# Performance work log

Measured on AMD Instinct MI355X. Metric: run time of the kernel, lower is better.

Reference implementation:

```python
import jax, jax.numpy as jnp
import numpy as np

NUM_EMBEDDINGS = 1024
EMBEDDING_DIM = 64

def setup_inputs() -> dict:
    key = jax.random.key(0)
    k1, k2 = jax.random.split(key)
    x = jax.random.normal(k1, (16, 64, 64, EMBEDDING_DIM), dtype=jnp.float32)
    # tf.random_uniform_initializer default: U(-0.05, 0.05)
    embeddings = jax.random.uniform(k2, (EMBEDDING_DIM, NUM_EMBEDDINGS),
                                    dtype=jnp.float32, minval=-0.05, maxval=0.05)
    return {"x": x, "embeddings": embeddings}

def reference(x, embeddings):
    input_shape = x.shape
    D = embeddings.shape[0]
    flat = x.reshape(-1, D)  # [N, D]
    # squared L2 distances: ||z||^2 + ||e||^2 - 2 z.e
    similarity = flat @ embeddings  # [N, K]
    distances = (jnp.sum(flat * flat, axis=1, keepdims=True)
                 + jnp.sum(embeddings * embeddings, axis=0)
                 - 2.0 * similarity)
    indices = jnp.argmin(distances, axis=1)  # [N]
    # one-hot @ embeddings.T == gather rows of embeddings.T
    quantized = jnp.take(embeddings.T, indices, axis=0)  # [N, D]
    return quantized.reshape(input_shape)
```

## Files before the change

### kernel.cpp

```cpp
#include <hip/hip_runtime.h>
#include <float.h>

#define K_CODES 1024
#define DIM 64
#define BR 128
#define SAFE_MARGIN 2.5e-4f

typedef __attribute__((ext_vector_type(8))) short bf16x8;
typedef __attribute__((ext_vector_type(8))) unsigned short u16x8;
typedef __attribute__((ext_vector_type(4))) float f32x4;

__device__ __forceinline__ unsigned short f2bf(float f) {
    unsigned int u = __float_as_uint(f);
    u += 0x7fff + ((u >> 16) & 1);
    return (unsigned short)(u >> 16);
}
__device__ __forceinline__ float bf2f(unsigned short h) {
    return __uint_as_float(((unsigned int)h) << 16);
}
__device__ __forceinline__ int swz(int row, int byteInRow) {
    return row * 128 + (byteInRow ^ ((row & 7) << 4));
}

__global__ __launch_bounds__(256) void vq_prep2(
    const float* __restrict__ E, float* __restrict__ Et,
    unsigned short* __restrict__ Eh, unsigned short* __restrict__ El,
    float* __restrict__ nrm, int* __restrict__ cnt)
{
    __shared__ float T[64 * 17];
    const int t = threadIdx.x;
    const int k0 = blockIdx.x * 16;
    if (blockIdx.x == 0 && t == 0) *cnt = 0;
    #pragma unroll
    for (int i = 0; i < 4; ++i) {
        int idx = i * 256 + t;
        int d = idx >> 4, kk = idx & 15;
        T[d * 17 + kk] = E[d * K_CODES + k0 + kk];
    }
    __syncthreads();
    #pragma unroll
    for (int i = 0; i < 4; ++i) {
        int idx = i * 256 + t;
        int kk = idx >> 6, d = idx & 63;
        float v = T[d * 17 + kk];
        Et[(size_t)(k0 + kk) * DIM + d] = v;
        unsigned short h = f2bf(v);
        Eh[(size_t)(k0 + kk) * DIM + d] = h;
        El[(size_t)(k0 + kk) * DIM + d] = f2bf(v - bf2f(h));
    }
    if (t < 16) {
        float s = 0.f;
        #pragma unroll
        for (int d = 0; d < DIM; ++d) {
            float v = T[d * 17 + t];
            s = __builtin_fmaf(v, v, s);
        }
        nrm[k0 + t] = s;
    }
}

__global__ __launch_bounds__(256, 2) void vq_mfma(
    const float* __restrict__ x,
    const unsigned short* __restrict__ Eh,
    const unsigned short* __restrict__ El,
    const float* __restrict__ nrm,
    const float* __restrict__ Et,
    float* __restrict__ out,
    int* __restrict__ cnt, int* __restrict__ list)
{
    __shared__ char lds[66048];
    char* Ah = lds;
    char* Al = lds + 16384;
    char* Bh = lds + 32768;
    char* Bl = lds + 49152;
    int* bidx = (int*)(lds + 65536);

    const int t    = threadIdx.x;
    const int lane = t & 63;
    const int wv   = t >> 6;
    const int col  = lane & 15;
    const int q    = lane >> 4;
    const int koff = q * 16;
    const long r0  = (long)blockIdx.x * BR;

    {
        int row = t >> 1, h = t & 1;
        const float4* src = (const float4*)(x + (r0 + row) * DIM + h * 32);
        float v[32];
        #pragma unroll
        for (int i = 0; i < 8; ++i) {
            float4 f = src[i];
            v[4*i+0] = f.x; v[4*i+1] = f.y; v[4*i+2] = f.z; v[4*i+3] = f.w;
        }
        unsigned short hi[32], lo[32];
        #pragma unroll
        for (int i = 0; i < 32; ++i) {
            hi[i] = f2bf(v[i]);
            lo[i] = f2bf(v[i] - bf2f(hi[i]));
        }
        #pragma unroll
        for (int s = 0; s < 2; ++s) {
            int seg = h * 2 + s;
            *(u16x8*)(Ah + swz(row, seg*32))      = *(u16x8*)(hi + s*16);
            *(u16x8*)(Ah + swz(row, seg*32 + 16)) = *(u16x8*)(hi + s*16 + 8);
            *(u16x8*)(Al + swz(row, seg*32))      = *(u16x8*)(lo + s*16);
            *(u16x8*)(Al + swz(row, seg*32 + 16)) = *(u16x8*)(lo + s*16 + 8);
        }
    }
    __syncthreads();

    bf16x8 aH[2][2], aL[2][2];
    #pragma unroll
    for (int m = 0; m < 2; ++m) {
        int arow = wv * 32 + m * 16 + col;
        #pragma unroll
        for (int kk = 0; kk < 2; ++kk) {
            aH[m][kk] = *(bf16x8*)(Ah + swz(arow, kk*64 + koff));
            aL[m][kk] = *(bf16x8*)(Al + swz(arow, kk*64 + koff));
        }
    }

    float b1[2][4], b2[2][4];
    int   i1[2][4];
    #pragma unroll
    for (int m = 0; m < 2; ++m)
        #pragma unroll
        for (int j = 0; j < 4; ++j) { b1[m][j] = FLT_MAX; b2[m][j] = FLT_MAX; i1[m][j] = 0x7fffffff; }

    for (int c0 = 0; c0 < K_CODES; c0 += 128) {
        __syncthreads();
        #pragma unroll
        for (int i = 0; i < 4; ++i) {
            int idx = i * 256 + t;
            int cr = idx >> 3, sg = idx & 7;
            *(u16x8*)(Bh + swz(cr, sg*16)) = *(const u16x8*)(Eh + (size_t)(c0+cr)*DIM + sg*8);
            *(u16x8*)(Bl + swz(cr, sg*16)) = *(const u16x8*)(El + (size_t)(c0+cr)*DIM + sg*8);
        }
        __syncthreads();

        #pragma unroll
        for (int nt = 0; nt < 8; ++nt) {
            int brow = nt * 16 + col;
            bf16x8 bH0 = *(bf16x8*)(Bh + swz(brow, koff));
            bf16x8 bH1 = *(bf16x8*)(Bh + swz(brow, 64 + koff));
            bf16x8 bL0 = *(bf16x8*)(Bl + swz(brow, koff));
            bf16x8 bL1 = *(bf16x8*)(Bl + swz(brow, 64 + koff));
            int code = c0 + nt * 16 + col;
            float ne = nrm[code];
            #pragma unroll
            for (int m = 0; m < 2; ++m) {
                f32x4 acc = {0.f, 0.f, 0.f, 0.f};
                acc = __builtin_amdgcn_mfma_f32_16x16x32_bf16(aH[m][0], bH0, acc, 0,0,0);
                acc = __builtin_amdgcn_mfma_f32_16x16x32_bf16(aH[m][1], bH1, acc, 0,0,0);
                acc = __builtin_amdgcn_mfma_f32_16x16x32_bf16(aH[m][0], bL0, acc, 0,0,0);
                acc = __builtin_amdgcn_mfma_f32_16x16x32_bf16(aH[m][1], bL1, acc, 0,0,0);
                acc = __builtin_amdgcn_mfma_f32_16x16x32_bf16(aL[m][0], bH0, acc, 0,0,0);
                acc = __builtin_amdgcn_mfma_f32_16x16x32_bf16(aL[m][1], bH1, acc, 0,0,0);
                #pragma unroll
                for (int j = 0; j < 4; ++j) {
                    float dist = __builtin_fmaf(-2.f, acc[j], ne);
                    if (dist < b1[m][j]) { b2[m][j] = b1[m][j]; b1[m][j] = dist; i1[m][j] = code; }
                    else if (dist < b2[m][j]) { b2[m][j] = dist; }
                }
            }
        }
    }

    #pragma unroll
    for (int msk = 1; msk < 16; msk <<= 1) {
        #pragma unroll
        for (int m = 0; m < 2; ++m)
            #pragma unroll
            for (int j = 0; j < 4; ++j) {
                float o1 = __shfl_xor(b1[m][j], msk, 64);
                int   oi = __shfl_xor(i1[m][j], msk, 64);
                float o2 = __shfl_xor(b2[m][j], msk, 64);
                bool take = (o1 < b1[m][j]) || (o1 == b1[m][j] && oi < i1[m][j]);
                float worst = take ? b1[m][j] : o1;
                if (take) { b1[m][j] = o1; i1[m][j] = oi; }
                b2[m][j] = fminf(fminf(b2[m][j], o2), worst);
            }
    }
    if (col == 0) {
        #pragma unroll
        for (int m = 0; m < 2; ++m)
            #pragma unroll
            for (int j = 0; j < 4; ++j) {
                int rowl = wv * 32 + m * 16 + q * 4 + j;
                bidx[rowl] = i1[m][j];
                if (b2[m][j] - b1[m][j] <= SAFE_MARGIN) {
                    int p = atomicAdd(cnt, 1);
                    list[p] = (int)(r0 + rowl);
                }
            }
    }
    __syncthreads();

    {
        int rowl = t >> 1, h = t & 1;
        int code = bidx[rowl];
        const float4* src = (const float4*)(Et + (size_t)code * DIM + h * 32);
        float4* dst = (float4*)(out + (size_t)(r0 + rowl) * DIM + h * 32);
        #pragma unroll
        for (int i = 0; i < 8; ++i) dst[i] = src[i];
    }
}

__global__ __launch_bounds__(256) void vq_refine3(
    const float* __restrict__ x, const float* __restrict__ Et,
    const float* __restrict__ nrm, float* __restrict__ out,
    const int* __restrict__ cnt, const int* __restrict__ list)
{
    __shared__ float zsh[DIM];
    __shared__ float rv[4];
    __shared__ int   ri[4];
    __shared__ int   winner;
    const int n = *cnt;
    const int t = threadIdx.x;
    const int lane = t & 63, wv = t >> 6;

    for (int i = blockIdx.x; i < n; i += gridDim.x) {
        int row = list[i];
        if (t < DIM) zsh[t] = x[(size_t)row * DIM + t];
        __syncthreads();

        float zn = 0.f;
        #pragma unroll
        for (int d = 0; d < DIM; ++d) zn = __builtin_fmaf(zsh[d], zsh[d], zn);

        const float* e0 = Et + (size_t)(t      ) * DIM;
        const float* e1 = Et + (size_t)(t + 256) * DIM;
        const float* e2 = Et + (size_t)(t + 512) * DIM;
        const float* e3 = Et + (size_t)(t + 768) * DIM;
        float a0 = 0.f, a1 = 0.f, a2 = 0.f, a3 = 0.f;
        #pragma unroll
        for (int d = 0; d < DIM; ++d) {
            float zd = zsh[d];
            a0 = __builtin_fmaf(zd, e0[d], a0);
            a1 = __builtin_fmaf(zd, e1[d], a1);
            a2 = __builtin_fmaf(zd, e2[d], a2);
            a3 = __builtin_fmaf(zd, e3[d], a3);
        }
        float d0 = __builtin_fmaf(-2.f, a0, zn + nrm[t      ]);
        float d1 = __builtin_fmaf(-2.f, a1, zn + nrm[t + 256]);
        float d2 = __builtin_fmaf(-2.f, a2, zn + nrm[t + 512]);
        float d3 = __builtin_fmaf(-2.f, a3, zn + nrm[t + 768]);

        float b1 = d0; int i1v = t;
        if (d1 < b1) { b1 = d1; i1v = t + 256; }
        if (d2 < b1) { b1 = d2; i1v = t + 512; }
        if (d3 < b1) { b1 = d3; i1v = t + 768; }

        #pragma unroll
        for (int m = 1; m < 64; m <<= 1) {
            float o1 = __shfl_xor(b1, m, 64);
            int   oi = __shfl_xor(i1v, m, 64);
            if (o1 < b1 || (o1 == b1 && oi < i1v)) { b1 = o1; i1v = oi; }
        }
        if (lane == 0) { rv[wv] = b1; ri[wv] = i1v; }
        __syncthreads();
        if (t == 0) {
            float bv = rv[0]; int bi = ri[0];
            #pragma unroll
            for (int w = 1; w < 4; ++w)
                if (rv[w] < bv || (rv[w] == bv && ri[w] < bi)) { bv = rv[w]; bi = ri[w]; }
            winner = bi;
        }
        __syncthreads();
        if (t < DIM) out[(size_t)row * DIM + t] = Et[(size_t)winner * DIM + t];
        __syncthreads();
    }
}

extern "C" void kernel_launch(void* const* d_in, const int* in_sizes, int n_in,
                              void* d_out, int out_size, void* d_ws, size_t ws_size,
                              hipStream_t stream) {
    const float* x = (const float*)d_in[0];
    const float* E = (const float*)d_in[1];
    float* out = (float*)d_out;

    char* ws = (char*)d_ws;
    float*          Et   = (float*)ws;
    unsigned short* Eh   = (unsigned short*)(ws + 262144);
    unsigned short* El   = (unsigned short*)(ws + 393216);
    float*          nrm  = (float*)(ws + 524288);
    int*            cnt  = (int*)(ws + 528384);
    int*            list = (int*)(ws + 528640);

    int nrows = in_sizes[0] / DIM;

    vq_prep2<<<64, 256, 0, stream>>>(E, Et, Eh, El, nrm, cnt);
    vq_mfma<<<nrows / BR, 256, 0, stream>>>(x, Eh, El, nrm, Et, out, cnt, list);
    vq_refine3<<<512, 256, 0, stream>>>(x, Et, nrm, out, cnt, list);
}
```

Before: 131.2 us.

## Fuse refinement into MFMA kernel, alias LDS buffers, fold norm into accumulator

Removes the separate refine kernel and the global atomic list. Each block now keeps a per-block list of ambiguous rows in LDS and re-scores them in fp32 at the end. The B tiles reuse the A tile LDS space, halving shared memory so launch bounds can allow 4 blocks per CU, which needs a barrier reorganisation. The accumulator is seeded with half the code norm and x is negated, so the distance comes straight out of the MFMA, and the top-2 tracking uses fmin/fmed3 without branches. The risk is that a few blocks doing serial refinement become tail stragglers.

```diff
diff --git a/kernel.cpp b/kernel.cpp
--- a/kernel.cpp
+++ b/kernel.cpp
@@ -4,7 +4,7 @@
 #define K_CODES 1024
 #define DIM 64
 #define BR 128
-#define SAFE_MARGIN 2.5e-4f
+#define SAFE_MARGIN_H 1.25e-4f
 
 typedef __attribute__((ext_vector_type(8))) short bf16x8;
 typedef __attribute__((ext_vector_type(8))) unsigned short u16x8;
@@ -25,12 +25,11 @@
 __global__ __launch_bounds__(256) void vq_prep2(
     const float* __restrict__ E, float* __restrict__ Et,
     unsigned short* __restrict__ Eh, unsigned short* __restrict__ El,
-    float* __restrict__ nrm, int* __restrict__ cnt)
+    float* __restrict__ nrm, float* __restrict__ nrm2)
 {
     __shared__ float T[64 * 17];
     const int t = threadIdx.x;
     const int k0 = blockIdx.x * 16;
-    if (blockIdx.x == 0 && t == 0) *cnt = 0;
     #pragma unroll
     for (int i = 0; i < 4; ++i) {
         int idx = i * 256 + t;
@@ -55,25 +54,29 @@
             float v = T[d * 17 + t];
             s = __builtin_fmaf(v, v, s);
         }
-        nrm[k0 + t] = s;
-    }
-}
-
-__global__ __launch_bounds__(256, 2) void vq_mfma(
+        nrm [k0 + t] = s;
+        nrm2[k0 + t] = 0.5f * s;
+    }
+}
+
+__global__ __launch_bounds__(256, 4) void vq_mfma(
     const float* __restrict__ x,
+    const float* __restrict__ E,
     const unsigned short* __restrict__ Eh,
     const unsigned short* __restrict__ El,
     const float* __restrict__ nrm,
+    const float* __restrict__ nrm2,
     const float* __restrict__ Et,
-    float* __restrict__ out,
-    int* __restrict__ cnt, int* __restrict__ list)
+    float* __restrict__ out)
 {
-    __shared__ char lds[66048];
+    __shared__ char lds[32768 + 512 + 512 + 16];
     char* Ah = lds;
     char* Al = lds + 16384;
-    char* Bh = lds + 32768;
-    char* Bl = lds + 49152;
-    int* bidx = (int*)(lds + 65536);
+    char* Bh = lds;
+    char* Bl = lds + 16384;
+    int*  bidx  = (int*)(lds + 32768);
+    int*  flist = (int*)(lds + 33280);
+    int*  fcnt  = (int*)(lds + 33792);
 
     const int t    = threadIdx.x;
     const int lane = t & 63;
@@ -83,6 +86,8 @@
     const int koff = q * 16;
     const long r0  = (long)blockIdx.x * BR;
 
+    if (t == 0) *fcnt = 0;
+
     {
         int row = t >> 1, h = t & 1;
         const float4* src = (const float4*)(x + (r0 + row) * DIM + h * 32);
@@ -90,7 +95,7 @@
         #pragma unroll
         for (int i = 0; i < 8; ++i) {
             float4 f = src[i];
-            v[4*i+0] = f.x; v[4*i+1] = f.y; v[4*i+2] = f.z; v[4*i+3] = f.w;
+            v[4*i+0] = -f.x; v[4*i+1] = -f.y; v[4*i+2] = -f.z; v[4*i+3] = -f.w;
         }
         unsigned short hi[32], lo[32];
         #pragma unroll
@@ -119,6 +124,7 @@
             aL[m][kk] = *(bf16x8*)(Al + swz(arow, kk*64 + koff));
         }
     }
+    __syncthreads();
 
     float b1[2][4], b2[2][4];
     int   i1[2][4];
@@ -128,7 +134,6 @@
         for (int j = 0; j < 4; ++j) { b1[m][j] = FLT_MAX; b2[m][j] = FLT_MAX; i1[m][j] = 0x7fffffff; }
 
     for (int c0 = 0; c0 < K_CODES; c0 += 128) {
-        __syncthreads();
         #pragma unroll
         for (int i = 0; i < 4; ++i) {
             int idx = i * 256 + t;
@@ -146,10 +151,10 @@
             bf16x8 bL0 = *(bf16x8*)(Bl + swz(brow, koff));
             bf16x8 bL1 = *(bf16x8*)(Bl + swz(brow, 64 + koff));
             int code = c0 + nt * 16 + col;
-            float ne = nrm[code];
+            float ne2 = nrm2[code];
             #pragma unroll
             for (int m = 0; m < 2; ++m) {
-                f32x4 acc = {0.f, 0.f, 0.f, 0.f};
+                f32x4 acc = {ne2, ne2, ne2, ne2};
                 acc = __builtin_amdgcn_mfma_f32_16x16x32_bf16(aH[m][0], bH0, acc, 0,0,0);
                 acc = __builtin_amdgcn_mfma_f32_16x16x32_bf16(aH[m][1], bH1, acc, 0,0,0);
                 acc = __builtin_amdgcn_mfma_f32_16x16x32_bf16(aH[m][0], bL0, acc, 0,0,0);
@@ -158,12 +163,16 @@
                 acc = __builtin_amdgcn_mfma_f32_16x16x32_bf16(aL[m][1], bH1, acc, 0,0,0);
                 #pragma unroll
                 for (int j = 0; j < 4; ++j) {
-                    float dist = __builtin_fmaf(-2.f, acc[j], ne);
-                    if (dist < b1[m][j]) { b2[m][j] = b1[m][j]; b1[m][j] = dist; i1[m][j] = code; }
-                    else if (dist < b2[m][j]) { b2[m][j] = dist; }
+                    float d = acc[j];
+                    bool lt = d < b1[m][j];
+                    float nb1 = fminf(b1[m][j], d);
+                    b2[m][j] = __builtin_amdgcn_fmed3f(b1[m][j], b2[m][j], d);
+                    i1[m][j] = lt ? code : i1[m][j];
+                    b1[m][j] = nb1;
                 }
             }
         }
+        __syncthreads();
     }
 
     #pragma unroll
@@ -188,9 +197,9 @@
             for (int j = 0; j < 4; ++j) {
                 int rowl = wv * 32 + m * 16 + q * 4 + j;
                 bidx[rowl] = i1[m][j];
-                if (b2[m][j] - b1[m][j] <= SAFE_MARGIN) {
-                    int p = atomicAdd(cnt, 1);
-                    list[p] = (int)(r0 + rowl);
+                if (b2[m][j] - b1[m][j] <= SAFE_MARGIN_H) {
+                    int p = atomicAdd(fcnt, 1);
+                    flist[p] = rowl;
                 }
             }
     }
@@ -204,71 +213,58 @@
         #pragma unroll
         for (int i = 0; i < 8; ++i) dst[i] = src[i];
     }
-}
-
-__global__ __launch_bounds__(256) void vq_refine3(
-    const float* __restrict__ x, const float* __restrict__ Et,
-    const float* __restrict__ nrm, float* __restrict__ out,
-    const int* __restrict__ cnt, const int* __restrict__ list)
-{
-    __shared__ float zsh[DIM];
-    __shared__ float rv[4];
-    __shared__ int   ri[4];
-    __shared__ int   winner;
-    const int n = *cnt;
-    const int t = threadIdx.x;
-    const int lane = t & 63, wv = t >> 6;
-
-    for (int i = blockIdx.x; i < n; i += gridDim.x) {
-        int row = list[i];
-        if (t < DIM) zsh[t] = x[(size_t)row * DIM + t];
-        __syncthreads();
-
-        float zn = 0.f;
-        #pragma unroll
-        for (int d = 0; d < DIM; ++d) zn = __builtin_fmaf(zsh[d], zsh[d], zn);
-
-        const float* e0 = Et + (size_t)(t      ) * DIM;
-        const float* e1 = Et + (size_t)(t + 256) * DIM;
-        const float* e2 = Et + (size_t)(t + 512) * DIM;
-        const float* e3 = Et + (size_t)(t + 768) * DIM;
-        float a0 = 0.f, a1 = 0.f, a2 = 0.f, a3 = 0.f;
-        #pragma unroll
-        for (int d = 0; d < DIM; ++d) {
-            float zd = zsh[d];
-            a0 = __builtin_fmaf(zd, e0[d], a0);
-            a1 = __builtin_fmaf(zd, e1[d], a1);
-            a2 = __builtin_fmaf(zd, e2[d], a2);
-            a3 = __builtin_fmaf(zd, e3[d], a3);
-        }
-        float d0 = __builtin_fmaf(-2.f, a0, zn + nrm[t      ]);
-        float d1 = __builtin_fmaf(-2.f, a1, zn + nrm[t + 256]);
-        float d2 = __builtin_fmaf(-2.f, a2, zn + nrm[t + 512]);
-        float d3 = __builtin_fmaf(-2.f, a3, zn + nrm[t + 768]);
-
-        float b1 = d0; int i1v = t;
-        if (d1 < b1) { b1 = d1; i1v = t + 256; }
-        if (d2 < b1) { b1 = d2; i1v = t + 512; }
-        if (d3 < b1) { b1 = d3; i1v = t + 768; }
-
-        #pragma unroll
-        for (int m = 1; m < 64; m <<= 1) {
-            float o1 = __shfl_xor(b1, m, 64);
-            int   oi = __shfl_xor(i1v, m, 64);
-            if (o1 < b1 || (o1 == b1 && oi < i1v)) { b1 = o1; i1v = oi; }
-        }
-        if (lane == 0) { rv[wv] = b1; ri[wv] = i1v; }
-        __syncthreads();
-        if (t == 0) {
-            float bv = rv[0]; int bi = ri[0];
-            #pragma unroll
-            for (int w = 1; w < 4; ++w)
-                if (rv[w] < bv || (rv[w] == bv && ri[w] < bi)) { bv = rv[w]; bi = ri[w]; }
-            winner = bi;
-        }
-        __syncthreads();
-        if (t < DIM) out[(size_t)row * DIM + t] = Et[(size_t)winner * DIM + t];
-        __syncthreads();
+    __syncthreads();
+
+    const int nf = *fcnt;
+    if (nf > 0) {
+        float* zsh    = (float*)lds;
+        float* rv     = (float*)(lds + 1024);
+        int*   ri     = (int*)  (lds + 1088);
+        int*   winner = (int*)  (lds + 1152);
+        for (int f = 0; f < nf; ++f) {
+            int rowl = flist[f];
+            if (t < DIM) zsh[t] = x[(r0 + rowl) * DIM + t];
+            __syncthreads();
+            float zn = 0.f;
+            #pragma unroll
+            for (int d = 0; d < DIM; ++d) zn = __builtin_fmaf(zsh[d], zsh[d], zn);
+            float a0 = 0.f, a1 = 0.f, a2 = 0.f, a3 = 0.f;
+            #pragma unroll
+            for (int d = 0; d < DIM; ++d) {
+                float zd = zsh[d];
+                const float* Ed = E + d * K_CODES;
+                a0 = __builtin_fmaf(zd, Ed[t      ], a0);
+                a1 = __builtin_fmaf(zd, Ed[t + 256], a1);
+                a2 = __builtin_fmaf(zd, Ed[t + 512], a2);
+                a3 = __builtin_fmaf(zd, Ed[t + 768], a3);
+            }
+            float d0 = __builtin_fmaf(-2.f, a0, zn + nrm[t      ]);
+            float d1 = __builtin_fmaf(-2.f, a1, zn + nrm[t + 256]);
+            float d2 = __builtin_fmaf(-2.f, a2, zn + nrm[t + 512]);
+            float d3 = __builtin_fmaf(-2.f, a3, zn + nrm[t + 768]);
+            float bv = d0; int bi = t;
+            if (d1 < bv) { bv = d1; bi = t + 256; }
+            if (d2 < bv) { bv = d2; bi = t + 512; }
+            if (d3 < bv) { bv = d3; bi = t + 768; }
+            #pragma unroll
+            for (int m = 1; m < 64; m <<= 1) {
+                float ov = __shfl_xor(bv, m, 64);
+                int   oi = __shfl_xor(bi, m, 64);
+                if (ov < bv || (ov == bv && oi < bi)) { bv = ov; bi = oi; }
+            }
+            if (lane == 0) { rv[wv] = bv; ri[wv] = bi; }
+            __syncthreads();
+            if (t == 0) {
+                float v = rv[0]; int b = ri[0];
+                #pragma unroll
+                for (int w = 1; w < 4; ++w)
+                    if (rv[w] < v || (rv[w] == v && ri[w] < b)) { v = rv[w]; b = ri[w]; }
+                *winner = b;
+            }
+            __syncthreads();
+            if (t < DIM) out[(r0 + rowl) * DIM + t] = Et[(size_t)(*winner) * DIM + t];
+            __syncthreads();
+        }
     }
 }
 
@@ -284,12 +280,10 @@
     unsigned short* Eh   = (unsigned short*)(ws + 262144);
     unsigned short* El   = (unsigned short*)(ws + 393216);
     float*          nrm  = (float*)(ws + 524288);
-    int*            cnt  = (int*)(ws + 528384);
-    int*            list = (int*)(ws + 528640);
+    float*          nrm2 = (float*)(ws + 528384);
 
     int nrows = in_sizes[0] / DIM;
 
-    vq_prep2<<<64, 256, 0, stream>>>(E, Et, Eh, El, nrm, cnt);
-    vq_mfma<<<nrows / BR, 256, 0, stream>>>(x, Eh, El, nrm, Et, out, cnt, list);
-    vq_refine3<<<512, 256, 0, stream>>>(x, Et, nrm, out, cnt, list);
-}
+    vq_prep2<<<64, 256, 0, stream>>>(E, Et, Eh, El, nrm, nrm2);
+    vq_mfma<<<nrows / BR, 256, 0, stream>>>(x, E, Eh, El, nrm, nrm2, Et, out);
+}
```

Result: slower. 197.6 us (+50.6%).
